# Kernel optimization log

Measured on AMD Instinct MI355X. Metric: run time of the kernel, lower is better.

Reference implementation:

```python
import jax, jax.numpy as jnp
import numpy as np

BATCH = 131072
INPUT_DIM = 256
HIDDEN = 128
DIM = 16
TRIL = DIM * (DIM + 1) // 2  # 136


def setup_inputs() -> dict:
    key = jax.random.key(0)
    k_x, k_w1, k_w2 = jax.random.split(key, 3)
    x = jax.random.normal(k_x, (BATCH, INPUT_DIM), dtype=jnp.float32)
    # Kaiming-ish init scaling so activations are well-conditioned
    W1 = jax.random.normal(k_w1, (INPUT_DIM, HIDDEN), dtype=jnp.float32) * (1.0 / np.sqrt(INPUT_DIM))
    b1 = jnp.zeros((HIDDEN,), dtype=jnp.float32)
    W2 = jax.random.normal(k_w2, (HIDDEN, TRIL), dtype=jnp.float32) * (1.0 / np.sqrt(HIDDEN))
    b2 = jnp.zeros((TRIL,), dtype=jnp.float32)
    return {"x": x, "W1": W1, "b1": b1, "W2": W2, "b2": b2}


def reference(x, W1, b1, W2, b2):
    # MLP: Linear -> ReLU -> Linear, producing tril entries of Cholesky factor
    h = jax.nn.relu(x @ W1 + b1)              # [B, 128]
    v = h @ W2 + b2                           # [B, 136]
    ti, tj = jnp.tril_indices(DIM)            # row-major tril order, matches torch.tril_indices
    L = jnp.zeros((x.shape[0], DIM, DIM), dtype=v.dtype).at[:, ti, tj].set(v)  # [B, D, D]
    rho = jnp.einsum('bik,bjk->bij', L, L)    # L @ L^T (real, so conj is no-op)
    trace = jnp.einsum('bii->b', rho)         # diagonal sum
    return rho / trace[:, None, None]
```

## Files before the change

### kernel.cpp

```cpp
#include <hip/hip_runtime.h>


typedef _Float16 h8 __attribute__((ext_vector_type(8)));
typedef float    f4 __attribute__((ext_vector_type(4)));
typedef int      i2 __attribute__((ext_vector_type(2)));

#define BATCH_N 131072
#define IN_DIM  256
#define HID     128
#define TRILN   136
#define BM      64
#define NT1     8
#define KS1     8
#define NT2     9
#define KS2     4
#define HSTR    136
#define LVSTR   160
#define CHUNKH  (16*LVSTR)
#define PW1_N   (KS1*NT1*64*8)
#define PW2_N   (KS2*NT2*64*8)

__device__ __forceinline__ int rowoff(int i) {
    int g = i >> 2;
    return 4 * (g + 1) * (2 * g + (i & 3));
}

__global__ void pack_weights(const float* __restrict__ W1,
                             const float* __restrict__ W2,
                             _Float16* __restrict__ pw1,
                             _Float16* __restrict__ pw2) {
    int gid = blockIdx.x * blockDim.x + threadIdx.x;
    if (gid < PW1_N) {
        int j = gid & 7, l = (gid >> 3) & 63, f = gid >> 9;
        int ks = f >> 3, nt = f & 7;
        int k = ks * 32 + (l >> 4) * 8 + j;
        int n = nt * 16 + (l & 15);
        pw1[gid] = (_Float16)W1[k * HID + n];
    } else if (gid < PW1_N + PW2_N) {
        int g = gid - PW1_N;
        int j = g & 7, l = (g >> 3) & 63, f = g >> 9;
        int ks = f / NT2, nt = f - ks * NT2;
        int k = ks * 32 + (l >> 4) * 8 + j;
        int col = nt * 16 + (l & 15);
        pw2[g] = (col < TRILN) ? (_Float16)W2[k * TRILN + col] : (_Float16)0.0f;
    }
}

__device__ __forceinline__ h8 cvt_h8(f4 lo, f4 hi) {
    h8 r;
    r[0] = (_Float16)lo[0]; r[1] = (_Float16)lo[1];
    r[2] = (_Float16)lo[2]; r[3] = (_Float16)lo[3];
    r[4] = (_Float16)hi[0]; r[5] = (_Float16)hi[1];
    r[6] = (_Float16)hi[2]; r[7] = (_Float16)hi[3];
    return r;
}

__global__ __launch_bounds__(256, 3) void fused_mlp(
        const float* __restrict__ x, const float* __restrict__ b1,
        const float* __restrict__ b2, const _Float16* __restrict__ pw1,
        const _Float16* __restrict__ pw2, float* __restrict__ out) {
    __shared__ _Float16 smem[4 * CHUNKH] __attribute__((aligned(16)));

    const int tid  = threadIdx.x;
    const int w    = tid >> 6;
    const int lane = tid & 63;
    const int q    = lane >> 4;
    const int lm   = lane & 15;
    const int b0   = blockIdx.x * BM;

    _Float16* hbuf = smem + w * CHUNKH;
    _Float16* lv   = smem + w * CHUNKH;

    const float* xp = x + (size_t)(b0 + w * 16 + lm) * IN_DIM + q * 8;
    f4 xa[2 * KS1];
    #pragma unroll
    for (int ks = 0; ks < KS1; ++ks) {
        xa[2 * ks]     = *(const f4*)(xp + ks * 32);
        xa[2 * ks + 1] = *(const f4*)(xp + ks * 32 + 4);
    }
    h8 xh[KS1];
    #pragma unroll
    for (int ks = 0; ks < KS1; ++ks)
        xh[ks] = cvt_h8(xa[2 * ks], xa[2 * ks + 1]);

    f4 acc1[NT1];
    #pragma unroll
    for (int nt = 0; nt < NT1; ++nt) acc1[nt] = (f4){0.f, 0.f, 0.f, 0.f};

    #pragma unroll
    for (int ks = 0; ks < KS1; ++ks) {
        h8 bf[NT1];
        #pragma unroll
        for (int nt = 0; nt < NT1; ++nt)
            bf[nt] = *(const h8*)(pw1 + ((ks * NT1 + nt) * 64 + lane) * 8);
        #pragma unroll
        for (int nt = 0; nt < NT1; ++nt)
            acc1[nt] = __builtin_amdgcn_mfma_f32_16x16x32_f16(xh[ks], bf[nt], acc1[nt], 0, 0, 0);
    }

    {
        float b1v[NT1];
        #pragma unroll
        for (int nt = 0; nt < NT1; ++nt) b1v[nt] = b1[nt * 16 + lm];
        #pragma unroll
        for (int nt = 0; nt < NT1; ++nt)
            #pragma unroll
            for (int r = 0; r < 4; ++r) {
                float hv = fmaxf(acc1[nt][r] + b1v[nt], 0.f);
                hbuf[(q * 4 + r) * HSTR + nt * 16 + lm] = (_Float16)hv;
            }
    }

    f4 acc2[NT2];
    #pragma unroll
    for (int nt = 0; nt < NT2; ++nt) acc2[nt] = (f4){0.f, 0.f, 0.f, 0.f};

    h8 ha[KS2];
    #pragma unroll
    for (int ks = 0; ks < KS2; ++ks)
        ha[ks] = *(const h8*)(hbuf + lm * HSTR + ks * 32 + q * 8);

    #pragma unroll
    for (int nt = 0; nt < NT2; ++nt) {
        #pragma unroll
        for (int ks = 0; ks < KS2; ++ks) {
            h8 bf = *(const h8*)(pw2 + ((ks * NT2 + nt) * 64 + lane) * 8);
            acc2[nt] = __builtin_amdgcn_mfma_f32_16x16x32_f16(ha[ks], bf, acc2[nt], 0, 0, 0);
        }
    }

    float b2v[NT2];
    #pragma unroll
    for (int nt = 0; nt < NT2; ++nt) {
        int col = nt * 16 + lm;
        b2v[nt] = (col < TRILN) ? b2[col] : 0.f;
    }

    float rinv[4];
    {
        float ps[4] = {0.f, 0.f, 0.f, 0.f};
        #pragma unroll
        for (int nt = 0; nt < NT2; ++nt)
            #pragma unroll
            for (int r = 0; r < 4; ++r) {
                float v = acc2[nt][r] + b2v[nt];
                ps[r] += v * v;
            }
        #pragma unroll
        for (int r = 0; r < 4; ++r) {
            float s = ps[r];
            s += __shfl_xor(s, 1);
            s += __shfl_xor(s, 2);
            s += __shfl_xor(s, 4);
            s += __shfl_xor(s, 8);
            rinv[r] = 1.0f / s;
        }
    }

    int voff[NT2];
    bool vok[NT2];
    #pragma unroll
    for (int nt = 0; nt < NT2; ++nt) {
        int c = nt * 16 + lm;
        vok[nt] = (c < TRILN);
        int cc = vok[nt] ? c : 0;
        int i = (int)((sqrtf(8.0f * (float)cc + 1.0f) - 1.0f) * 0.5f);
        int k = cc - (i * (i + 1)) / 2;
        voff[nt] = rowoff(i) + k;
    }

    #pragma unroll
    for (int r = 0; r < 4; ++r) {
        int base = (q * 4 + r) * LVSTR;
        #pragma unroll
        for (int nt = 0; nt < NT2; ++nt)
            if (vok[nt])
                lv[base + voff[nt]] = (_Float16)(acc2[nt][r] + b2v[nt]);
    }

    int msk[4];
    {
        int n = lm - q * 8 + 1;
        #pragma unroll
        for (int p = 0; p < 4; ++p) {
            int c2 = n - 2 * p; c2 = c2 < 0 ? 0 : (c2 > 2 ? 2 : c2);
            msk[p] = (c2 == 2) ? ~0 : ((c2 == 1) ? 0xFFFF : 0);
        }
    }
    const int ro_lm = rowoff(lm);
    const f4 zero = (f4){0.f, 0.f, 0.f, 0.f};
    const int outcol = q * 64 + lm;

    #pragma unroll
    for (int tq = 0; tq < 4; ++tq)
        #pragma unroll
        for (int r4 = 0; r4 < 4; ++r4) {
            int t = tq * 4 + r4;
            const _Float16* rp = lv + t * LVSTR + ro_lm + q * 8;
            i2 lo = *(const i2*)rp;
            i2 hi = *(const i2*)(rp + 4);
            h8 frag;
            ((i2*)&frag)[0] = (i2){lo.x & msk[0], lo.y & msk[1]};
            ((i2*)&frag)[1] = (i2){hi.x & msk[2], hi.y & msk[3]};
            f4 d = __builtin_amdgcn_mfma_f32_16x16x32_f16(frag, frag, zero, 0, 0, 0);
            float riv = __uint_as_float(
                __builtin_amdgcn_readlane(__float_as_uint(rinv[r4]), tq * 16));
            float* op = out + (size_t)(b0 + w * 16 + t) * 256 + outcol;
            #pragma unroll
            for (int sr = 0; sr < 4; ++sr)
                op[sr * 16] = d[sr] * riv;
        }
}

extern "C" void kernel_launch(void* const* d_in, const int* in_sizes, int n_in,
                              void* d_out, int out_size, void* d_ws, size_t ws_size,
                              hipStream_t stream) {
    const float* x  = (const float*)d_in[0];
    const float* W1 = (const float*)d_in[1];
    const float* b1 = (const float*)d_in[2];
    const float* W2 = (const float*)d_in[3];
    const float* b2 = (const float*)d_in[4];
    float* out = (float*)d_out;

    _Float16* pw1 = (_Float16*)d_ws;
    _Float16* pw2 = pw1 + PW1_N;

    pack_weights<<<(PW1_N + PW2_N + 255) / 256, 256, 0, stream>>>(W1, W2, pw1, pw2);
    fused_mlp<<<BATCH_N / BM, 256, 0, stream>>>(x, b1, b2, pw1, pw2, out);
}
```

Before: 264.9 us.

## Stage W1 in LDS with 1024-thread blocks processing two row tiles per wave

```diff
diff --git a/kernel.cpp b/kernel.cpp
--- a/kernel.cpp
+++ b/kernel.cpp
@@ -9,7 +9,6 @@
 #define IN_DIM  256
 #define HID     128
 #define TRILN   136
-#define BM      64
 #define NT1     8
 #define KS1     8
 #define NT2     9
@@ -19,6 +18,9 @@
 #define CHUNKH  (16*LVSTR)
 #define PW1_N   (KS1*NT1*64*8)
 #define PW2_N   (KS2*NT2*64*8)
+#define NWAVE   16
+#define ROWS_PER_BLOCK (NWAVE*32)
+#define LDS_BYTES (PW1_N*2 + NWAVE*CHUNKH*2)
 
 __device__ __forceinline__ int rowoff(int i) {
     int g = i >> 2;
@@ -55,107 +57,42 @@
     return r;
 }
 
-__global__ __launch_bounds__(256, 3) void fused_mlp(
+__global__ __launch_bounds__(1024, 4) void fused_mlp(
         const float* __restrict__ x, const float* __restrict__ b1,
         const float* __restrict__ b2, const _Float16* __restrict__ pw1,
         const _Float16* __restrict__ pw2, float* __restrict__ out) {
-    __shared__ _Float16 smem[4 * CHUNKH] __attribute__((aligned(16)));
+    extern __shared__ _Float16 smem[];
 
     const int tid  = threadIdx.x;
     const int w    = tid >> 6;
     const int lane = tid & 63;
     const int q    = lane >> 4;
     const int lm   = lane & 15;
-    const int b0   = blockIdx.x * BM;
-
-    _Float16* hbuf = smem + w * CHUNKH;
-    _Float16* lv   = smem + w * CHUNKH;
-
-    const float* xp = x + (size_t)(b0 + w * 16 + lm) * IN_DIM + q * 8;
+    const int rw0  = blockIdx.x * ROWS_PER_BLOCK + w * 32;
+
+    const _Float16* pwl = smem;
+    _Float16* chunk = smem + PW1_N + w * CHUNKH;
+    _Float16* hbuf = chunk;
+    _Float16* lv   = chunk;
+
+    const float* xp = x + (size_t)(rw0 + lm) * IN_DIM + q * 8;
     f4 xa[2 * KS1];
     #pragma unroll
     for (int ks = 0; ks < KS1; ++ks) {
         xa[2 * ks]     = *(const f4*)(xp + ks * 32);
         xa[2 * ks + 1] = *(const f4*)(xp + ks * 32 + 4);
     }
-    h8 xh[KS1];
-    #pragma unroll
-    for (int ks = 0; ks < KS1; ++ks)
-        xh[ks] = cvt_h8(xa[2 * ks], xa[2 * ks + 1]);
-
-    f4 acc1[NT1];
-    #pragma unroll
-    for (int nt = 0; nt < NT1; ++nt) acc1[nt] = (f4){0.f, 0.f, 0.f, 0.f};
-
-    #pragma unroll
-    for (int ks = 0; ks < KS1; ++ks) {
-        h8 bf[NT1];
-        #pragma unroll
-        for (int nt = 0; nt < NT1; ++nt)
-            bf[nt] = *(const h8*)(pw1 + ((ks * NT1 + nt) * 64 + lane) * 8);
-        #pragma unroll
-        for (int nt = 0; nt < NT1; ++nt)
-            acc1[nt] = __builtin_amdgcn_mfma_f32_16x16x32_f16(xh[ks], bf[nt], acc1[nt], 0, 0, 0);
-    }
 
     {
-        float b1v[NT1];
-        #pragma unroll
-        for (int nt = 0; nt < NT1; ++nt) b1v[nt] = b1[nt * 16 + lm];
-        #pragma unroll
-        for (int nt = 0; nt < NT1; ++nt)
-            #pragma unroll
-            for (int r = 0; r < 4; ++r) {
-                float hv = fmaxf(acc1[nt][r] + b1v[nt], 0.f);
-                hbuf[(q * 4 + r) * HSTR + nt * 16 + lm] = (_Float16)hv;
-            }
-    }
-
-    f4 acc2[NT2];
-    #pragma unroll
-    for (int nt = 0; nt < NT2; ++nt) acc2[nt] = (f4){0.f, 0.f, 0.f, 0.f};
-
-    h8 ha[KS2];
-    #pragma unroll
-    for (int ks = 0; ks < KS2; ++ks)
-        ha[ks] = *(const h8*)(hbuf + lm * HSTR + ks * 32 + q * 8);
-
-    #pragma unroll
-    for (int nt = 0; nt < NT2; ++nt) {
-        #pragma unroll
-        for (int ks = 0; ks < KS2; ++ks) {
-            h8 bf = *(const h8*)(pw2 + ((ks * NT2 + nt) * 64 + lane) * 8);
-            acc2[nt] = __builtin_amdgcn_mfma_f32_16x16x32_f16(ha[ks], bf, acc2[nt], 0, 0, 0);
-        }
-    }
-
-    float b2v[NT2];
-    #pragma unroll
-    for (int nt = 0; nt < NT2; ++nt) {
-        int col = nt * 16 + lm;
-        b2v[nt] = (col < TRILN) ? b2[col] : 0.f;
-    }
-
-    float rinv[4];
-    {
-        float ps[4] = {0.f, 0.f, 0.f, 0.f};
-        #pragma unroll
-        for (int nt = 0; nt < NT2; ++nt)
-            #pragma unroll
-            for (int r = 0; r < 4; ++r) {
-                float v = acc2[nt][r] + b2v[nt];
-                ps[r] += v * v;
-            }
-        #pragma unroll
-        for (int r = 0; r < 4; ++r) {
-            float s = ps[r];
-            s += __shfl_xor(s, 1);
-            s += __shfl_xor(s, 2);
-            s += __shfl_xor(s, 4);
-            s += __shfl_xor(s, 8);
-            rinv[r] = 1.0f / s;
-        }
-    }
+        const f4* src = (const f4*)pw1;
+        f4* dst = (f4*)smem;
+        #pragma unroll
+        for (int k = 0; k < 4; ++k) {
+            int i = k * 1024 + tid;
+            dst[i] = src[i];
+        }
+    }
+    __syncthreads();
 
     int voff[NT2];
     bool vok[NT2];
@@ -168,16 +105,6 @@
         int k = cc - (i * (i + 1)) / 2;
         voff[nt] = rowoff(i) + k;
     }
-
-    #pragma unroll
-    for (int r = 0; r < 4; ++r) {
-        int base = (q * 4 + r) * LVSTR;
-        #pragma unroll
-        for (int nt = 0; nt < NT2; ++nt)
-            if (vok[nt])
-                lv[base + voff[nt]] = (_Float16)(acc2[nt][r] + b2v[nt]);
-    }
-
     int msk[4];
     {
         int n = lm - q * 8 + 1;
@@ -192,24 +119,123 @@
     const int outcol = q * 64 + lm;
 
     #pragma unroll
-    for (int tq = 0; tq < 4; ++tq)
-        #pragma unroll
-        for (int r4 = 0; r4 < 4; ++r4) {
-            int t = tq * 4 + r4;
-            const _Float16* rp = lv + t * LVSTR + ro_lm + q * 8;
-            i2 lo = *(const i2*)rp;
-            i2 hi = *(const i2*)(rp + 4);
-            h8 frag;
-            ((i2*)&frag)[0] = (i2){lo.x & msk[0], lo.y & msk[1]};
-            ((i2*)&frag)[1] = (i2){hi.x & msk[2], hi.y & msk[3]};
-            f4 d = __builtin_amdgcn_mfma_f32_16x16x32_f16(frag, frag, zero, 0, 0, 0);
-            float riv = __uint_as_float(
-                __builtin_amdgcn_readlane(__float_as_uint(rinv[r4]), tq * 16));
-            float* op = out + (size_t)(b0 + w * 16 + t) * 256 + outcol;
-            #pragma unroll
-            for (int sr = 0; sr < 4; ++sr)
-                op[sr * 16] = d[sr] * riv;
-        }
+    for (int t = 0; t < 2; ++t) {
+        const int r0 = rw0 + t * 16;
+
+        h8 xh[KS1];
+        #pragma unroll
+        for (int ks = 0; ks < KS1; ++ks)
+            xh[ks] = cvt_h8(xa[2 * ks], xa[2 * ks + 1]);
+        if (t == 0) {
+            const float* xp1 = xp + (size_t)16 * IN_DIM;
+            #pragma unroll
+            for (int ks = 0; ks < KS1; ++ks) {
+                xa[2 * ks]     = *(const f4*)(xp1 + ks * 32);
+                xa[2 * ks + 1] = *(const f4*)(xp1 + ks * 32 + 4);
+            }
+        }
+
+        f4 acc1[NT1];
+        #pragma unroll
+        for (int nt = 0; nt < NT1; ++nt) acc1[nt] = (f4){0.f, 0.f, 0.f, 0.f};
+
+        #pragma unroll
+        for (int ks = 0; ks < KS1; ++ks) {
+            #pragma unroll
+            for (int nt = 0; nt < NT1; ++nt) {
+                h8 bf = *(const h8*)(pwl + ((ks * NT1 + nt) * 64 + lane) * 8);
+                acc1[nt] = __builtin_amdgcn_mfma_f32_16x16x32_f16(xh[ks], bf, acc1[nt], 0, 0, 0);
+            }
+        }
+
+        {
+            float b1v;
+            #pragma unroll
+            for (int nt = 0; nt < NT1; ++nt) {
+                b1v = b1[nt * 16 + lm];
+                #pragma unroll
+                for (int r = 0; r < 4; ++r) {
+                    float hv = fmaxf(acc1[nt][r] + b1v, 0.f);
+                    hbuf[(q * 4 + r) * HSTR + nt * 16 + lm] = (_Float16)hv;
+                }
+            }
+        }
+
+        f4 acc2[NT2];
+        #pragma unroll
+        for (int nt = 0; nt < NT2; ++nt) acc2[nt] = (f4){0.f, 0.f, 0.f, 0.f};
+
+        h8 ha[KS2];
+        #pragma unroll
+        for (int ks = 0; ks < KS2; ++ks)
+            ha[ks] = *(const h8*)(hbuf + lm * HSTR + ks * 32 + q * 8);
+
+        #pragma unroll
+        for (int nt = 0; nt < NT2; ++nt) {
+            #pragma unroll
+            for (int ks = 0; ks < KS2; ++ks) {
+                h8 bf = *(const h8*)(pw2 + ((ks * NT2 + nt) * 64 + lane) * 8);
+                acc2[nt] = __builtin_amdgcn_mfma_f32_16x16x32_f16(ha[ks], bf, acc2[nt], 0, 0, 0);
+            }
+        }
+
+        float b2v[NT2];
+        #pragma unroll
+        for (int nt = 0; nt < NT2; ++nt) {
+            int col = nt * 16 + lm;
+            b2v[nt] = (col < TRILN) ? b2[col] : 0.f;
+        }
+
+        float rinv[4];
+        {
+            float ps[4] = {0.f, 0.f, 0.f, 0.f};
+            #pragma unroll
+            for (int nt = 0; nt < NT2; ++nt)
+                #pragma unroll
+                for (int r = 0; r < 4; ++r) {
+                    float v = acc2[nt][r] + b2v[nt];
+                    ps[r] += v * v;
+                }
+            #pragma unroll
+            for (int r = 0; r < 4; ++r) {
+                float s = ps[r];
+                s += __shfl_xor(s, 1);
+                s += __shfl_xor(s, 2);
+                s += __shfl_xor(s, 4);
+                s += __shfl_xor(s, 8);
+                rinv[r] = 1.0f / s;
+            }
+        }
+
+        #pragma unroll
+        for (int r = 0; r < 4; ++r) {
+            int base = (q * 4 + r) * LVSTR;
+            #pragma unroll
+            for (int nt = 0; nt < NT2; ++nt)
+                if (vok[nt])
+                    lv[base + voff[nt]] = (_Float16)(acc2[nt][r] + b2v[nt]);
+        }
+
+        #pragma unroll
+        for (int tq = 0; tq < 4; ++tq)
+            #pragma unroll
+            for (int r4 = 0; r4 < 4; ++r4) {
+                int tt = tq * 4 + r4;
+                const _Float16* rp = lv + tt * LVSTR + ro_lm + q * 8;
+                i2 lo = *(const i2*)rp;
+                i2 hi = *(const i2*)(rp + 4);
+                h8 frag;
+                ((i2*)&frag)[0] = (i2){lo.x & msk[0], lo.y & msk[1]};
+                ((i2*)&frag)[1] = (i2){hi.x & msk[2], hi.y & msk[3]};
+                f4 d = __builtin_amdgcn_mfma_f32_16x16x32_f16(frag, frag, zero, 0, 0, 0);
+                float riv = __uint_as_float(
+                    __builtin_amdgcn_readlane(__float_as_uint(rinv[r4]), tq * 16));
+                float* op = out + (size_t)(r0 + tt) * 256 + outcol;
+                #pragma unroll
+                for (int sr = 0; sr < 4; ++sr)
+                    op[sr * 16] = d[sr] * riv;
+            }
+    }
 }
 
 extern "C" void kernel_launch(void* const* d_in, const int* in_sizes, int n_in,
@@ -225,6 +251,12 @@
     _Float16* pw1 = (_Float16*)d_ws;
     _Float16* pw2 = pw1 + PW1_N;
 
+    static int lds_ok = 0;
+    (void)hipFuncSetAttribute((const void*)fused_mlp,
+                              hipFuncAttributeMaxDynamicSharedMemorySize,
+                              LDS_BYTES);
+    (void)lds_ok;
+
     pack_weights<<<(PW1_N + PW2_N + 255) / 256, 256, 0, stream>>>(W1, W2, pw1, pw2);
-    fused_mlp<<<BATCH_N / BM, 256, 0, stream>>>(x, b1, b2, pw1, pw2, out);
-}
+    fused_mlp<<<BATCH_N / ROWS_PER_BLOCK, 1024, LDS_BYTES, stream>>>(x, b1, b2, pw1, pw2, out);
+}
```

After: 329.0 us. 24.2% more time.
